# Kernel tuning notes

Hardware: AMD Instinct MI355X
Metric: run time of the kernel (lower is better)

The kernel has to match this reference:

```python
import jax, jax.numpy as jnp
import numpy as np

B, C, H, W = 32, 64, 56, 56
REPN, NK, SMALL = 50, 17, 3   # repN=64-int(64*0.23), nk=ceil(51/3)
GROUPS = 4                     # N_rep
EPS = 1e-5


def _build_index_mats():
    """Reduce the fallback's python scatter-add loops to exact linear maps.
    For flat position p=r*NK+j the roll shifts depend only on p%3, so each
    shift class s gets a (REPN,NK) count matrix over source nk-slots."""
    rng = np.random.RandomState(123)
    ghost = np.sort(rng.choice(C, C - REPN, replace=False))
    rep = np.array(sorted(set(range(C)) - set(ghost.tolist())), np.int32)
    Mh = np.zeros((3, REPN, NK), np.int32)
    Mv = np.zeros((3, REPN, NK), np.int32)
    Mid = np.zeros((REPN, NK), np.int32)
    for _ in range(GROUPS):
        for r in range(REPN):
            perm = rng.permutation(NK)
            for p in range(NK):
                Mh[(r * NK + p) % 3, r, perm[p]] += 1
        for r in range(REPN):
            perm = rng.permutation(NK)
            for p in range(NK):
                Mv[(r * NK + p) % 3, r, perm[p]] += 1
        kk = rng.randint(0, NK, REPN)
        for r in range(REPN):
            Mid[r, kk[r]] += 1
    return ghost.astype(np.int32), rep, Mh, Mv, Mid


def setup_inputs() -> dict:
    key = jax.random.key(0)
    k1, k2, k3 = jax.random.split(key, 3)
    ghost, rep, Mh, Mv, Mid = _build_index_mats()
    return {
        "inputs": jax.random.normal(k1, (B, C, H, W), jnp.float32),
        "w0": jax.random.normal(k2, (REPN * NK, 1, SMALL, SMALL), jnp.float32) * 0.1,
        "w1": jax.random.normal(k3, (REPN * NK, 1, SMALL, SMALL), jnp.float32) * 0.1,
        "Mh": jnp.asarray(Mh), "Mv": jnp.asarray(Mv), "Mid": jnp.asarray(Mid),
        "ghost_idx": jnp.asarray(ghost), "rep_idx": jnp.asarray(rep),
    }


def _bn(x):
    # BatchNorm2d in training mode, affine weight=1 / bias=0 (init values)
    m = x.mean(axis=(0, 2, 3), keepdims=True)
    v = x.var(axis=(0, 2, 3), keepdims=True)
    return (x - m) / jnp.sqrt(v + EPS)


def reference(inputs, w0, w1, Mh, Mv, Mid, ghost_idx, rep_idx):
    rep_in = inputs[:, rep_idx]      # (B, REPN, H, W)
    ghost_in = inputs[:, ghost_idx]  # (B, ghostN, H, W)

    def conv(w):  # depthwise-grouped conv: groups=REPN, each 1->NK channels
        return jax.lax.conv_general_dilated(
            rep_in, w, window_strides=(1, 1), padding=((2, 2), (2, 2)),
            dimension_numbers=('NCHW', 'OIHW', 'NCHW'),
            feature_group_count=REPN)

    out = conv(w0) + conv(w1)                       # (B, REPN*NK, H+2, W+2)
    xv = out.reshape(B, REPN, NK, H + 2, W + 2)

    Mhf, Mvf, Midf = (m.astype(xv.dtype) for m in (Mh, Mv, Mid))
    sh1, sw1 = (0, 1, 2), (0, 2, 1)   # lora1: shifts (i%3, 2i%3)
    sh2, sw2 = (0, 2, 1), (0, 1, 2)   # lora2: shifts (2i%3, i%3)

    lora1 = sum(jnp.roll(jnp.einsum('rk,brkhw->brhw', Mhf[s], xv),
                         (sh1[s], sw1[s]), axis=(2, 3)) for s in range(3))
    lora2 = sum(jnp.roll(jnp.einsum('rk,brkhw->brhw', Mvf[s], xv),
                         (sh2[s], sw2[s]), axis=(2, 3)) for s in range(3))
    small = jnp.einsum('rk,brkhw->brhw', Midf, xv)

    # center-crop back to (H, W): dh = dw = 1
    lora1 = lora1[:, :, 1:1 + H, 1:1 + W]
    lora2 = lora2[:, :, 1:1 + H, 1:1 + W]
    small = small[:, :, 1:1 + H, 1:1 + W]

    x = _bn(lora1) + _bn(lora2) + _bn(small) + rep_in
    return jnp.concatenate([x, ghost_in], axis=1)   # (B, C, H, W)
```

## Files before the change

kernel.cpp:

```cpp
#include <hip/hip_runtime.h>

#define Bn 32
#define Cn 64
#define Hn 56
#define Wn 56
#define REPN 50
#define NKn 17
#define HWn (Hn*Wn)
#define NSTATf 100352.0f
#define EPSf 1e-5f

#define PART_OFF 0

#define SEGH 7
#define NTASK 112

__device__ __forceinline__ void block_weff(int r, int tid,
        const float* __restrict__ w0, const float* __restrict__ w1,
        const int* __restrict__ Mh, const int* __restrict__ Mv,
        const int* __restrict__ Mid, float* __restrict__ swk)
{
    if (tid < 63) {
        int t = tid / 9, ij = tid - t*9;
        const int* M = (t < 3) ? (Mh + (t*REPN + r)*NKn)
                     : (t < 6) ? (Mv + ((t-3)*REPN + r)*NKn)
                               : (Mid + r*NKn);
        float acc = 0.f;
        #pragma unroll
        for (int k = 0; k < NKn; ++k)
            acc += (float)M[k] * (w0[(r*NKn + k)*9 + ij] + w1[(r*NKn + k)*9 + ij]);
        swk[t*9 + ij] = acc;
    }
}

__device__ __forceinline__ void load_row8c(const float* __restrict__ ch, int row, int q,
                                           float* __restrict__ X, float& c55)
{
    bool rv = (row >= 0) && (row < Hn);
    int rc = rv ? row : 0;
    const float* rp = ch + rc*Wn;
    float4 c0 = *(const float4*)(rp + (q ? 4*q - 4 : 0));
    float4 c1 = *(const float4*)(rp + 4*q);
    int ox = (4*q + 4 <= 55) ? 4*q + 4 : 55;
    float cx = rp[ox];
    float mr = rv ? 1.f : 0.f;
    float m0 = (rv && q > 0)  ? 1.f : 0.f;
    float mx = (rv && q < 13) ? 1.f : 0.f;
    X[0]=c0.y*m0; X[1]=c0.z*m0; X[2]=c0.w*m0;
    X[3]=c1.x*mr; X[4]=c1.y*mr; X[5]=c1.z*mr; X[6]=c1.w*mr;
    X[7]=cx*mx;
    c55 = (q == 0) ? rp[55]*mr : 0.f;
}

template <typename F>
__device__ __forceinline__ void conv_walk3(const float* __restrict__ ch,
        const float (&wk)[63], int tid, F emit)
{
    if (tid >= NTASK) return;
    int seg = tid / 14;
    int q   = tid - seg*14;
    int h0  = seg * SEGH;
    bool top = (seg == 0);

    float W[6][8], C[6], T[8];
    {
        float dummy;
        if (top) load_row8c(ch, 55, q, T, dummy);
    }
    #pragma unroll
    for (int k = 0; k < 6; ++k)
        load_row8c(ch, h0 - 3 + k, q, W[k], C[k]);

    #pragma unroll
    for (int s = 0; s < SEGH; ++s) {
        int h = h0 + s;
        float Wn8[8], Cn1;
        load_row8c(ch, h + 3, q, Wn8, Cn1);

        float l1[4], l2[4], sm[4];
        #pragma unroll
        for (int p = 0; p < 4; ++p) { l1[p]=0.f; l2[p]=0.f; sm[p]=0.f; }
        #pragma unroll
        for (int i = 0; i < 3; ++i)
            #pragma unroll
            for (int j = 0; j < 3; ++j) {
                int ij = i*3 + j;
                float wh0 = wk[ij],    wh1 = wk[9+ij],  wh2 = wk[18+ij];
                float wv0 = wk[27+ij], wv1 = wk[36+ij], wv2 = wk[45+ij];
                float wid = wk[54+ij];
                #pragma unroll
                for (int p = 0; p < 4; ++p) {
                    float a  = W[2+i][p+2+j];
                    l1[p] = fmaf(a, wh0, l1[p]);
                    l2[p] = fmaf(a, wv0, l2[p]);
                    sm[p] = fmaf(a, wid, sm[p]);
                    float bA = W[1+i][p+j];
                    l1[p] = fmaf(bA, wh1, l1[p]);
                    l2[p] = fmaf(bA, wv2, l2[p]);
                    float bB = W[i][p+1+j];
                    l1[p] = fmaf(bB, wh2, l1[p]);
                    l2[p] = fmaf(bB, wv1, l2[p]);
                }
            }
        if (q == 0) {
            #pragma unroll
            for (int i = 0; i < 3; ++i) {
                l1[0] = fmaf(C[1+i], wk[9+3*i],  l1[0]);
                l2[0] = fmaf(C[1+i], wk[45+3*i], l2[0]);
            }
        }
        if (s == 0 && top) {
            #pragma unroll
            for (int j = 0; j < 3; ++j)
                #pragma unroll
                for (int p = 0; p < 4; ++p) {
                    l1[p] = fmaf(T[p+1+j], wk[18+j], l1[p]);
                    l2[p] = fmaf(T[p+1+j], wk[36+j], l2[p]);
                }
        }
        float res[4] = {W[3][3], W[3][4], W[3][5], W[3][6]};
        emit(h, q, l1, l2, sm, res);

        #pragma unroll
        for (int k = 0; k < 5; ++k) {
            #pragma unroll
            for (int x = 0; x < 8; ++x) W[k][x] = W[k+1][x];
            C[k] = C[k+1];
        }
        #pragma unroll
        for (int x = 0; x < 8; ++x) W[5][x] = Wn8[x];
        C[5] = Cn1;
    }
}

__device__ __forceinline__ void conv_walk1(const float* __restrict__ ch,
        const float (&cw0)[9], const float (&cwA)[9], const float (&cwB)[9],
        float Kc, int tid, float* __restrict__ dst)
{
    if (tid >= NTASK) return;
    int seg = tid / 14;
    int q   = tid - seg*14;
    int h0  = seg * SEGH;
    bool top = (seg == 0);

    float W[6][8], C[6], T[8];
    {
        float dummy;
        if (top) load_row8c(ch, 55, q, T, dummy);
    }
    #pragma unroll
    for (int k = 0; k < 6; ++k)
        load_row8c(ch, h0 - 3 + k, q, W[k], C[k]);

    #pragma unroll
    for (int s = 0; s < SEGH; ++s) {
        int h = h0 + s;
        float Wn8[8], Cn1;
        load_row8c(ch, h + 3, q, Wn8, Cn1);

        float acc[4];
        #pragma unroll
        for (int p = 0; p < 4; ++p) acc[p] = 0.f;
        #pragma unroll
        for (int i = 0; i < 3; ++i)
            #pragma unroll
            for (int j = 0; j < 3; ++j) {
                int ij = i*3 + j;
                float w0c = cw0[ij], wAc = cwA[ij], wBc = cwB[ij];
                #pragma unroll
                for (int p = 0; p < 4; ++p) {
                    acc[p] = fmaf(W[2+i][p+2+j], w0c, acc[p]);
                    acc[p] = fmaf(W[1+i][p+j],   wAc, acc[p]);
                    acc[p] = fmaf(W[i][p+1+j],   wBc, acc[p]);
                }
            }
        if (q == 0) {
            #pragma unroll
            for (int i = 0; i < 3; ++i)
                acc[0] = fmaf(C[1+i], cwA[3*i], acc[0]);
        }
        if (s == 0 && top) {
            #pragma unroll
            for (int j = 0; j < 3; ++j)
                #pragma unroll
                for (int p = 0; p < 4; ++p)
                    acc[p] = fmaf(T[p+1+j], cwB[j], acc[p]);
        }
        float4 o;
        o.x = acc[0] - Kc + W[3][3];
        o.y = acc[1] - Kc + W[3][4];
        o.z = acc[2] - Kc + W[3][5];
        o.w = acc[3] - Kc + W[3][6];
        *(float4*)(dst + h*Wn + 4*q) = o;

        #pragma unroll
        for (int k = 0; k < 5; ++k) {
            #pragma unroll
            for (int x = 0; x < 8; ++x) W[k][x] = W[k+1][x];
            C[k] = C[k+1];
        }
        #pragma unroll
        for (int x = 0; x < 8; ++x) W[5][x] = Wn8[x];
        C[5] = Cn1;
    }
}

__global__ void __launch_bounds__(128) k_pass1(const float* __restrict__ in,
        const float* __restrict__ w0, const float* __restrict__ w1,
        const int* __restrict__ Mh, const int* __restrict__ Mv,
        const int* __restrict__ Mid,
        const int* __restrict__ rep_idx, float* __restrict__ ws)
{
    int bid = blockIdx.x;
    int r = bid % REPN;
    int b = bid / REPN;
    int tid = threadIdx.x;

    __shared__ float swk[63];
    __shared__ float red[2][6];

    block_weff(r, tid, w0, w1, Mh, Mv, Mid, swk);
    __syncthreads();
    float wk[63];
    #pragma unroll
    for (int i = 0; i < 63; ++i) wk[i] = swk[i];

    const float* ch = in + ((size_t)(b*Cn + rep_idx[r]))*HWn;

    float s1=0.f,q1=0.f,s2=0.f,q2=0.f,s3=0.f,q3=0.f;
    conv_walk3(ch, wk, tid,
        [&](int h, int q, float* l1, float* l2, float* sm, float* res) {
            (void)h; (void)q; (void)res;
            #pragma unroll
            for (int p = 0; p < 4; ++p) {
                s1 += l1[p]; q1 += l1[p]*l1[p];
                s2 += l2[p]; q2 += l2[p]*l2[p];
                s3 += sm[p]; q3 += sm[p]*sm[p];
            }
        });

    float vals[6] = {s1,q1,s2,q2,s3,q3};
    int lane = tid & 63, wave = tid >> 6;
    #pragma unroll
    for (int x = 0; x < 6; ++x) {
        float y = vals[x];
        for (int o = 32; o; o >>= 1) y += __shfl_down(y, o, 64);
        if (lane == 0) red[wave][x] = y;
    }
    __syncthreads();
    if (tid < 6)
        ws[PART_OFF + (tid*REPN + r)*Bn + b] = red[0][tid] + red[1][tid];
}

__global__ void __launch_bounds__(128) k_pass2(const float* __restrict__ in,
        const float* __restrict__ w0, const float* __restrict__ w1,
        const int* __restrict__ Mh, const int* __restrict__ Mv,
        const int* __restrict__ Mid,
        const int* __restrict__ rep_idx, const int* __restrict__ ghost_idx,
        const float* __restrict__ ws, float* __restrict__ out)
{
    int bid = blockIdx.x;
    int c = bid & 63;
    int b = bid >> 6;
    int tid = threadIdx.x;

    if (c >= REPN) {
        int cin = ghost_idx[c - REPN];
        const float4* s4 = (const float4*)(in + ((size_t)(b*Cn + cin))*HWn);
        float4* d4 = (float4*)(out + ((size_t)(b*Cn + c))*HWn);
        for (int i = tid; i < HWn/4; i += 128) d4[i] = s4[i];
        return;
    }
    int r = c;

    __shared__ float swk[63];
    __shared__ float sred[6];

    block_weff(r, tid, w0, w1, Mh, Mv, Mid, swk);
    if (tid >= 64 && tid < 70) {
        int x = tid - 64;
        const float* pp = ws + PART_OFF + (x*REPN + r)*Bn;
        float s = 0.f;
        #pragma unroll
        for (int i = 0; i < Bn; ++i) s += pp[i];
        sred[x] = s;
    }
    __syncthreads();

    const float inv = 1.0f / NSTATf;
    float m1 = sred[0]*inv, v1 = sred[1]*inv - m1*m1;
    float m2 = sred[2]*inv, v2 = sred[3]*inv - m2*m2;
    float m3 = sred[4]*inv, v3 = sred[5]*inv - m3*m3;
    float r1 = rsqrtf(v1 + EPSf), r2 = rsqrtf(v2 + EPSf), r3 = rsqrtf(v3 + EPSf);
    float Kc = m1*r1 + m2*r2 + m3*r3;

    float cw0[9], cwA[9], cwB[9];
    #pragma unroll
    for (int ij = 0; ij < 9; ++ij) {
        cw0[ij] = r1*swk[ij]      + r2*swk[27+ij] + r3*swk[54+ij];
        cwA[ij] = r1*swk[9+ij]    + r2*swk[45+ij];
        cwB[ij] = r1*swk[18+ij]   + r2*swk[36+ij];
    }

    const float* ch = in + ((size_t)(b*Cn + rep_idx[r]))*HWn;
    float* dst = out + ((size_t)(b*Cn + c))*HWn;
    conv_walk1(ch, cw0, cwA, cwB, Kc, tid, dst);
}

extern "C" void kernel_launch(void* const* d_in, const int* in_sizes, int n_in,
                              void* d_out, int out_size, void* d_ws, size_t ws_size,
                              hipStream_t stream) {
    const float* in   = (const float*)d_in[0];
    const float* w0   = (const float*)d_in[1];
    const float* w1   = (const float*)d_in[2];
    const int*   Mh   = (const int*)d_in[3];
    const int*   Mv   = (const int*)d_in[4];
    const int*   Mid  = (const int*)d_in[5];
    const int*   ghost= (const int*)d_in[6];
    const int*   rep  = (const int*)d_in[7];
    float* out  = (float*)d_out;
    float* ws   = (float*)d_ws;

    k_pass1<<<REPN*Bn, 128, 0, stream>>>(in, w0, w1, Mh, Mv, Mid, rep, ws);
    k_pass2<<<Bn*Cn,   128, 0, stream>>>(in, w0, w1, Mh, Mv, Mid, rep, ghost, ws, out);
}
```

Before: 119.7 us.

## Fuse stats and output passes into one persistent kernel with atomic grid barrier

Replaces the two-kernel scheme (stats pass, then normalize/output pass) with one fused kernel of 1024 blocks. Each block handles two rep channels for one batch, accumulates BN statistics with global atomics, then spins on a per-channel arrival counter before writing the normalized output. Ghost channels are copied by otherwise idle blocks. This removes the second launch and keeps the input tile warm in cache, but adds a memset, an occupancy query on the host, and relies on all blocks being co-resident to avoid deadlock, with contention on the spin waits.

```diff
diff --git a/kernel.cpp b/kernel.cpp
--- a/kernel.cpp
+++ b/kernel.cpp
@@ -10,17 +10,21 @@
 #define NSTATf 100352.0f
 #define EPSf 1e-5f
 
-#define PART_OFF 0
+#define GCNT_OFF 0
+#define GSUM_OFF 1600
+#define INIT_BYTES 8000
+#define PART_OFF 4096
 
 #define SEGH 7
 #define NTASK 112
+#define GRID_FUSED 1024
 
 __device__ __forceinline__ void block_weff(int r, int tid,
         const float* __restrict__ w0, const float* __restrict__ w1,
         const int* __restrict__ Mh, const int* __restrict__ Mv,
         const int* __restrict__ Mid, float* __restrict__ swk)
 {
-    if (tid < 63) {
+    if (tid >= 0 && tid < 63) {
         int t = tid / 9, ij = tid - t*9;
         const int* M = (t < 3) ? (Mh + (t*REPN + r)*NKn)
                      : (t < 6) ? (Mv + ((t-3)*REPN + r)*NKn)
@@ -205,27 +209,13 @@
     }
 }
 
-__global__ void __launch_bounds__(128) k_pass1(const float* __restrict__ in,
-        const float* __restrict__ w0, const float* __restrict__ w1,
-        const int* __restrict__ Mh, const int* __restrict__ Mv,
-        const int* __restrict__ Mid,
-        const int* __restrict__ rep_idx, float* __restrict__ ws)
-{
-    int bid = blockIdx.x;
-    int r = bid % REPN;
-    int b = bid / REPN;
-    int tid = threadIdx.x;
-
-    __shared__ float swk[63];
-    __shared__ float red[2][6];
-
-    block_weff(r, tid, w0, w1, Mh, Mv, Mid, swk);
-    __syncthreads();
+__device__ __forceinline__ void stats_and_arrive(const float* __restrict__ ch,
+        const float* __restrict__ swk, int r, int tid,
+        float* __restrict__ ws, float (*red)[6])
+{
     float wk[63];
     #pragma unroll
     for (int i = 0; i < 63; ++i) wk[i] = swk[i];
-
-    const float* ch = in + ((size_t)(b*Cn + rep_idx[r]))*HWn;
 
     float s1=0.f,q1=0.f,s2=0.f,q2=0.f,s3=0.f,q3=0.f;
     conv_walk3(ch, wk, tid,
@@ -238,6 +228,136 @@
                 s3 += sm[p]; q3 += sm[p]*sm[p];
             }
         });
+    {
+        float vals[6] = {s1,q1,s2,q2,s3,q3};
+        int lane = tid & 63, wave = tid >> 6;
+        #pragma unroll
+        for (int x = 0; x < 6; ++x) {
+            float y = vals[x];
+            for (int o = 32; o; o >>= 1) y += __shfl_down(y, o, 64);
+            if (lane == 0) red[wave][x] = y;
+        }
+    }
+    __syncthreads();
+    if (tid < 6) {
+        atomicAdd(ws + GSUM_OFF + r*8 + tid, red[0][tid] + red[1][tid]);
+        __threadfence();
+    }
+    __syncthreads();
+    if (tid == 0)
+        atomicAdd(((unsigned*)ws) + GCNT_OFF + r*32, 1u);
+    __syncthreads();
+}
+
+__device__ __forceinline__ void wait_and_finalize(const float* __restrict__ ch,
+        const float* __restrict__ swk, int r, int tid,
+        float* __restrict__ ws, float* __restrict__ sred,
+        float* __restrict__ dst)
+{
+    if (tid == 0) {
+        unsigned* gc = ((unsigned*)ws) + GCNT_OFF + r*32;
+        while (atomicAdd(gc, 0u) < (unsigned)Bn)
+            __builtin_amdgcn_s_sleep(8);
+    }
+    __syncthreads();
+    if (tid < 6) sred[tid] = atomicAdd(ws + GSUM_OFF + r*8 + tid, 0.f);
+    __syncthreads();
+
+    const float inv = 1.0f / NSTATf;
+    float m1 = sred[0]*inv, v1 = sred[1]*inv - m1*m1;
+    float m2 = sred[2]*inv, v2 = sred[3]*inv - m2*m2;
+    float m3 = sred[4]*inv, v3 = sred[5]*inv - m3*m3;
+    float r1 = rsqrtf(v1 + EPSf), r2 = rsqrtf(v2 + EPSf), r3 = rsqrtf(v3 + EPSf);
+    float Kc = m1*r1 + m2*r2 + m3*r3;
+
+    float cw0[9], cwA[9], cwB[9];
+    #pragma unroll
+    for (int ij = 0; ij < 9; ++ij) {
+        cw0[ij] = r1*swk[ij]    + r2*swk[27+ij] + r3*swk[54+ij];
+        cwA[ij] = r1*swk[9+ij]  + r2*swk[45+ij];
+        cwB[ij] = r1*swk[18+ij] + r2*swk[36+ij];
+    }
+    conv_walk1(ch, cw0, cwA, cwB, Kc, tid, dst);
+}
+
+__global__ void __launch_bounds__(128) k_fused(const float* __restrict__ in,
+        const float* __restrict__ w0, const float* __restrict__ w1,
+        const int* __restrict__ Mh, const int* __restrict__ Mv,
+        const int* __restrict__ Mid,
+        const int* __restrict__ rep_idx, const int* __restrict__ ghost_idx,
+        float* __restrict__ ws, float* __restrict__ out)
+{
+    int tid = threadIdx.x;
+    int bid = blockIdx.x;
+    int b   = bid >> 5;
+    int pr  = bid & 31;
+    int cA  = 2*pr, cB = 2*pr + 1;
+
+    if (pr >= REPN/2) {
+        #pragma unroll
+        for (int it = 0; it < 2; ++it) {
+            int c = cA + it;
+            int cin = ghost_idx[c - REPN];
+            const float4* s4 = (const float4*)(in + ((size_t)(b*Cn + cin))*HWn);
+            float4* d4 = (float4*)(out + ((size_t)(b*Cn + c))*HWn);
+            for (int i = tid; i < HWn/4; i += 128) d4[i] = s4[i];
+        }
+        return;
+    }
+
+    __shared__ float swkA[63], swkB[63];
+    __shared__ float red[2][6];
+    __shared__ float sredA[6], sredB[6];
+
+    block_weff(cA, tid,      w0, w1, Mh, Mv, Mid, swkA);
+    block_weff(cB, tid - 64, w0, w1, Mh, Mv, Mid, swkB);
+    __syncthreads();
+
+    const float* chA = in + ((size_t)(b*Cn + rep_idx[cA]))*HWn;
+    const float* chB = in + ((size_t)(b*Cn + rep_idx[cB]))*HWn;
+
+    stats_and_arrive(chA, swkA, cA, tid, ws, red);
+    stats_and_arrive(chB, swkB, cB, tid, ws, red);
+
+    float* dstA = out + ((size_t)(b*Cn + cA))*HWn;
+    float* dstB = out + ((size_t)(b*Cn + cB))*HWn;
+    wait_and_finalize(chA, swkA, cA, tid, ws, sredA, dstA);
+    wait_and_finalize(chB, swkB, cB, tid, ws, sredB, dstB);
+}
+
+__global__ void __launch_bounds__(128) k_pass1(const float* __restrict__ in,
+        const float* __restrict__ w0, const float* __restrict__ w1,
+        const int* __restrict__ Mh, const int* __restrict__ Mv,
+        const int* __restrict__ Mid,
+        const int* __restrict__ rep_idx, float* __restrict__ ws)
+{
+    int bid = blockIdx.x;
+    int r = bid % REPN;
+    int b = bid / REPN;
+    int tid = threadIdx.x;
+
+    __shared__ float swk[63];
+    __shared__ float red[2][6];
+
+    block_weff(r, tid, w0, w1, Mh, Mv, Mid, swk);
+    __syncthreads();
+    float wk[63];
+    #pragma unroll
+    for (int i = 0; i < 63; ++i) wk[i] = swk[i];
+
+    const float* ch = in + ((size_t)(b*Cn + rep_idx[r]))*HWn;
+
+    float s1=0.f,q1=0.f,s2=0.f,q2=0.f,s3=0.f,q3=0.f;
+    conv_walk3(ch, wk, tid,
+        [&](int h, int q, float* l1, float* l2, float* sm, float* res) {
+            (void)h; (void)q; (void)res;
+            #pragma unroll
+            for (int p = 0; p < 4; ++p) {
+                s1 += l1[p]; q1 += l1[p]*l1[p];
+                s2 += l2[p]; q2 += l2[p]*l2[p];
+                s3 += sm[p]; q3 += sm[p]*sm[p];
+            }
+        });
 
     float vals[6] = {s1,q1,s2,q2,s3,q3};
     int lane = tid & 63, wave = tid >> 6;
@@ -297,9 +417,9 @@
     float cw0[9], cwA[9], cwB[9];
     #pragma unroll
     for (int ij = 0; ij < 9; ++ij) {
-        cw0[ij] = r1*swk[ij]      + r2*swk[27+ij] + r3*swk[54+ij];
-        cwA[ij] = r1*swk[9+ij]    + r2*swk[45+ij];
-        cwB[ij] = r1*swk[18+ij]   + r2*swk[36+ij];
+        cw0[ij] = r1*swk[ij]    + r2*swk[27+ij] + r3*swk[54+ij];
+        cwA[ij] = r1*swk[9+ij]  + r2*swk[45+ij];
+        cwB[ij] = r1*swk[18+ij] + r2*swk[36+ij];
     }
 
     const float* ch = in + ((size_t)(b*Cn + rep_idx[r]))*HWn;
@@ -321,6 +441,19 @@
     float* out  = (float*)d_out;
     float* ws   = (float*)d_ws;
 
+    int maxBlk = 0;
+    hipError_t qerr = hipOccupancyMaxActiveBlocksPerMultiprocessor(
+        &maxBlk, (const void*)k_fused, 128, 0);
+    bool fused_ok = (qerr == hipSuccess) && (maxBlk >= 4);
+
+    if (fused_ok) {
+        hipError_t merr = hipMemsetAsync(ws, 0, INIT_BYTES, stream);
+        if (merr == hipSuccess) {
+            k_fused<<<GRID_FUSED, 128, 0, stream>>>(in, w0, w1, Mh, Mv, Mid,
+                                                    rep, ghost, ws, out);
+            return;
+        }
+    }
     k_pass1<<<REPN*Bn, 128, 0, stream>>>(in, w0, w1, Mh, Mv, Mid, rep, ws);
     k_pass2<<<Bn*Cn,   128, 0, stream>>>(in, w0, w1, Mh, Mv, Mid, rep, ghost, ws, out);
 }
```

After: 118.3 us, median of 2. No clear change (-1.2%).
